# Kernel tuning notes

Hardware: AMD Instinct MI355X
Metric: run time of the kernel (lower is better)

## Reference

```python
import jax, jax.numpy as jnp
import numpy as np

B, NUM, NVAR = 2048, 100, 11
NUM_OBS, NC = 10, 3
T_FIN = 10.0
RHO_OBS = 1.0; RHO_INEQ = 1.0; RHO_LANE = 1.0; RHO_PROJ = 1.0
W_SMOOTH = 20.0; W_VDES = 2.0; W_YDES = 1.0
A_EGO = 3.0; B_EGO = 1.5; MARGIN = 0.2
V_MIN = 0.001; V_MAX = 18.0; A_MAX = 6.0
MAXITER = 5
H = 256

def _basis():
    s = np.linspace(0.0, 1.0, NUM)
    j = np.arange(NVAR)
    P = s[:, None] ** j[None, :]
    Pd = np.zeros((NUM, NVAR)); Pdd = np.zeros((NUM, NVAR))
    Pd[:, 1:] = j[1:][None, :] * s[:, None] ** (j[1:] - 1)[None, :]
    Pdd[:, 2:] = (j[2:] * (j[2:] - 1))[None, :] * s[:, None] ** (j[2:] - 2)[None, :]
    return (jnp.asarray(P, jnp.float32), jnp.asarray(Pd / T_FIN, jnp.float32),
            jnp.asarray(Pdd / (T_FIN ** 2), jnp.float32))

P, PDOT, PDDOT = _basis()
A_EQ_X = jnp.stack([P[0], PDOT[0], PDDOT[0], P[-1]])   # [4, NVAR]
A_EQ_Y = jnp.stack([P[0], PDOT[0], PDDOT[0]])          # [3, NVAR]
PTP = P.T @ P

def _kkt_inv(Q, A):
    m = A.shape[0]
    K = jnp.concatenate([jnp.concatenate([Q, A.T], axis=1),
                         jnp.concatenate([A, jnp.zeros((m, m), jnp.float32)], axis=1)], axis=0)
    return jnp.linalg.inv(K)

# ADMM cost: rho_proj*I + smoothness + rho_obs*A_obs^T A_obs + rho_ineq*(Pdot^T Pdot + Pddot^T Pddot)
Q_COMMON = (RHO_PROJ + W_SMOOTH) * jnp.eye(NVAR, dtype=jnp.float32) \
    + RHO_OBS * NUM_OBS * NC * PTP \
    + RHO_INEQ * (PDOT.T @ PDOT + PDDOT.T @ PDDOT)
KKT_X = _kkt_inv(Q_COMMON, A_EQ_X)
KKT_Y = _kkt_inv(Q_COMMON + 2.0 * RHO_LANE * PTP, A_EQ_Y)   # A_lane = [P; -P]
# x_init QP (smoothness + v_des / y_des tracking)
Q_IX = W_SMOOTH * jnp.eye(NVAR, dtype=jnp.float32) + W_VDES * (PDOT.T @ PDOT)
KKT_IX = _kkt_inv(Q_IX, A_EQ_X)
KKT_IY = _kkt_inv(Q_IX + W_YDES * PTP, A_EQ_Y)


def _forward(init_state_ego, goal_des, closest_obs, psi_obs, dim_x_obs, dim_y_obs,
             y_ub, y_lb, gru_W_ih, gru_W_hh, gru_b, gru_h0,
             mlp_W1, mlp_b1, mlp_W2, mlp_b2):
    b = init_state_ego.shape[0]
    x0, y0, vx0, vy0, ax0, ay0 = (init_state_ego[:, i] for i in range(6))
    b_eq_x = jnp.stack([x0, vx0, ax0, goal_des[:, 0]], axis=1)   # [B,4]
    b_eq_y = jnp.stack([y0, vy0, ay0], axis=1)                    # [B,3]

    # ---- obstacle circle trajectories (static obstacles, vx=vy=0) ----
    xo = closest_obs[:, :NUM_OBS]; yo = closest_obs[:, NUM_OBS:2 * NUM_OBS]   # [B,O]
    r = jnp.stack([jnp.zeros_like(dim_x_obs),
                   (dim_x_obs - dim_y_obs) / 2,
                   -(dim_x_obs - dim_y_obs) / 2], axis=2)                      # [B,O,3]
    x_circ = xo[:, :, None] + r * jnp.cos(psi_obs)[:, :, None]                # [B,O,3]
    y_circ = yo[:, :, None] + r * jnp.sin(psi_obs)[:, :, None]
    shape4 = (b, NUM_OBS, NC, NUM)
    x_obs_f = jnp.broadcast_to(x_circ[..., None], shape4).reshape(b, -1)      # [B,O*C*T]
    y_obs_f = jnp.broadcast_to(y_circ[..., None], shape4).reshape(b, -1)
    rad = dim_y_obs / 2
    a_obs = jnp.broadcast_to((A_EGO + rad + MARGIN)[:, :, None, None], shape4).reshape(b, -1)
    b_obs = jnp.broadcast_to((B_EGO + rad + MARGIN)[:, :, None, None], shape4).reshape(b, -1)

    # ---- GRU context over obstacles -> learned lambda init ----
    feats = jnp.stack([xo, yo, dim_x_obs, dim_y_obs, psi_obs], axis=2)        # [B,O,5]
    def gru_step(h, x):
        gx = x @ gru_W_ih + gru_b
        gh = h @ gru_W_hh
        z = jax.nn.sigmoid(gx[:, :H] + gh[:, :H])
        rg = jax.nn.sigmoid(gx[:, H:2 * H] + gh[:, H:2 * H])
        n = jnp.tanh(gx[:, 2 * H:] + rg * gh[:, 2 * H:])
        return (1.0 - z) * n + z * h, None
    hT, _ = jax.lax.scan(gru_step, jnp.broadcast_to(gru_h0, (b, H)), jnp.swapaxes(feats, 0, 1))
    lam = jax.nn.relu(hT @ mlp_W1 + mlp_b1) @ mlp_W2 + mlp_b2                 # [B,2*NVAR]
    lam_x, lam_y = lam[:, :NVAR], lam[:, NVAR:]

    # ---- x_init: equality-constrained smoothness/tracking QP ----
    v_des = jnp.sqrt(vx0 ** 2 + vy0 ** 2)
    lin_ix = W_VDES * v_des[:, None] * jnp.sum(PDOT, axis=0)[None, :]
    lin_iy = W_YDES * goal_des[:, 1:2] * jnp.sum(P, axis=0)[None, :]
    c_x0 = (jnp.concatenate([lin_ix, b_eq_x], 1) @ KKT_IX.T)[:, :NVAR]
    c_y0 = (jnp.concatenate([lin_iy, b_eq_y], 1) @ KKT_IY.T)[:, :NVAR]

    b_lane = jnp.concatenate([y_ub[:, None] * jnp.ones((1, NUM), jnp.float32),
                              -y_lb[:, None] * jnp.ones((1, NUM), jnp.float32)], axis=1)  # [B,2T]

    def AobsT(v):   # A_obs^T v, v: [B, O*C*T] -> [B, NVAR]
        return v.reshape(b, NUM_OBS * NC, NUM).sum(axis=1) @ P

    def step(carry, _):
        c_x, c_y, lx, ly = carry
        x = c_x @ P.T; xd = c_x @ PDOT.T; xdd = c_x @ PDDOT.T
        y = c_y @ P.T; yd = c_y @ PDOT.T; ydd = c_y @ PDDOT.T
        wc = jnp.tile(x, (1, NUM_OBS * NC)) - x_obs_f
        ws = jnp.tile(y, (1, NUM_OBS * NC)) - y_obs_f
        alpha_o = jnp.arctan2(ws * a_obs, wc * b_obs)
        ca, sa = jnp.cos(alpha_o), jnp.sin(alpha_o)
        c1 = RHO_OBS * (a_obs ** 2 * ca ** 2 + b_obs ** 2 * sa ** 2)
        c2 = RHO_OBS * (a_obs * wc * ca + b_obs * ws * sa)
        d_o = jnp.maximum(1.0, c2 / c1)
        alpha_v = jnp.clip(jnp.arctan2(yd, xd), -0.41, 0.41)
        cv, sv = jnp.cos(alpha_v), jnp.sin(alpha_v)
        d_v = jnp.clip(xd * cv + yd * sv, V_MIN, V_MAX)
        alpha_a = jnp.arctan2(ydd + 1e-4, xdd + 1e-4)
        caa, saa = jnp.cos(alpha_a), jnp.sin(alpha_a)
        d_a = jnp.clip(xdd * caa + ydd * saa, 0.0, A_MAX)
        # targets
        b_ox = x_obs_f + a_obs * d_o * ca; b_oy = y_obs_f + b_obs * d_o * sa
        b_vx = d_v * cv; b_vy = d_v * sv
        b_ax = d_a * caa; b_ay = d_a * saa
        b_lane_aug = jnp.minimum(jnp.concatenate([y, -y], 1), b_lane)  # slack-augmented
        top_x = lx + RHO_PROJ * c_x0 + RHO_OBS * AobsT(b_ox) + RHO_INEQ * (b_vx @ PDOT + b_ax @ PDDOT)
        top_y = ly + RHO_PROJ * c_y0 + RHO_OBS * AobsT(b_oy) + RHO_INEQ * (b_vy @ PDOT + b_ay @ PDDOT) \
            + RHO_LANE * ((b_lane_aug[:, :NUM] - b_lane_aug[:, NUM:]) @ P)
        c_xn = (jnp.concatenate([top_x, b_eq_x], 1) @ KKT_X.T)[:, :NVAR]
        c_yn = (jnp.concatenate([top_y, b_eq_y], 1) @ KKT_Y.T)[:, :NVAR]
        # residuals / Lagrange multiplier updates
        xn = c_xn @ P.T; yn = c_yn @ P.T
        res_ox = jnp.tile(xn, (1, NUM_OBS * NC)) - b_ox
        res_oy = jnp.tile(yn, (1, NUM_OBS * NC)) - b_oy
        lxn = lx - RHO_OBS * AobsT(res_ox) \
            - RHO_INEQ * ((c_xn @ PDOT.T - b_vx) @ PDOT + (c_xn @ PDDOT.T - b_ax) @ PDDOT)
        res_lane = jnp.concatenate([yn, -yn], 1) - b_lane_aug
        lyn = ly - RHO_OBS * AobsT(res_oy) \
            - RHO_INEQ * ((c_yn @ PDOT.T - b_vy) @ PDOT + (c_yn @ PDDOT.T - b_ay) @ PDDOT) \
            - RHO_LANE * ((res_lane[:, :NUM] - res_lane[:, NUM:]) @ P)
        return (c_xn, c_yn, lxn, lyn), None

    (c_x, c_y, lam_x, lam_y), _ = jax.lax.scan(step, (c_x0, c_y0, lam_x, lam_y),
                                               None, length=MAXITER)
    return jnp.concatenate([c_x, c_y], axis=1)   # [B, 2*NVAR]


def setup_inputs() -> dict:
    key = jax.random.key(0)
    ks = jax.random.split(key, 12)
    d = {
        'init_state_ego': jax.random.normal(ks[0], (B, 6), jnp.float32),
        'goal_des': jax.random.normal(ks[1], (B, 2), jnp.float32),
        'closest_obs': jax.random.normal(ks[2], (B, 2 * NUM_OBS), jnp.float32),
        'psi_obs': jax.random.normal(ks[3], (B, NUM_OBS), jnp.float32),
        'dim_x_obs': jax.random.uniform(ks[4], (B, NUM_OBS), jnp.float32),
        'dim_y_obs': jax.random.uniform(ks[5], (B, NUM_OBS), jnp.float32),
        'y_ub': jnp.ones((B,), jnp.float32),
        'y_lb': jnp.zeros((B,), jnp.float32),
        'gru_W_ih': jax.random.normal(ks[6], (5, 3 * H), jnp.float32) / np.sqrt(5.0),
        'gru_W_hh': jax.random.normal(ks[7], (H, 3 * H), jnp.float32) / np.sqrt(float(H)),
        'gru_b': jnp.zeros((3 * H,), jnp.float32),
        'gru_h0': jax.random.normal(ks[8], (H,), jnp.float32) * 0.1,
        'mlp_W1': jax.random.normal(ks[9], (H, 512), jnp.float32) / np.sqrt(float(H)),
        'mlp_b1': jnp.zeros((512,), jnp.float32),
        'mlp_W2': jax.random.normal(ks[10], (512, 2 * NVAR), jnp.float32) / np.sqrt(512.0),
        'mlp_b2': jnp.zeros((2 * NVAR,), jnp.float32),
    }
    return d


def reference(init_state_ego, goal_des, closest_obs, psi_obs, dim_x_obs, dim_y_obs,
              y_ub, y_lb, gru_W_ih, gru_W_hh, gru_b, gru_h0,
              mlp_W1, mlp_b1, mlp_W2, mlp_b2):
    return _forward(init_state_ego, goal_des, closest_obs, psi_obs, dim_x_obs, dim_y_obs,
                    y_ub, y_lb, gru_W_ih, gru_W_hh, gru_b, gru_h0,
                    mlp_W1, mlp_b1, mlp_W2, mlp_b2)
```

## Files before the change

### kernel.cpp

```cpp
#include <hip/hip_runtime.h>
#include <math.h>

typedef short bf16x8 __attribute__((ext_vector_type(8)));
typedef float f32x4 __attribute__((ext_vector_type(4)));

__device__ __forceinline__ unsigned short f2bf(float x) {
  union { float f; unsigned u; } v; v.f = x;
  unsigned r = v.u + 0x7FFFu + ((v.u >> 16) & 1u);
  return (unsigned short)(r >> 16);
}

#define WS_WAUG 0u
#define WS_W1T  442368u
#define WS_W2T  704512u
#define WS_LAM  737280u
#define WS_KKT  917504u
#define WS_SUMS 920320u

__global__ __launch_bounds__(256) void prep(
    const float* __restrict__ Whh, const float* __restrict__ Wih,
    const float* __restrict__ gb, const float* __restrict__ W1,
    const float* __restrict__ W2,
    unsigned short* __restrict__ Waug, unsigned short* __restrict__ W1T,
    unsigned short* __restrict__ W2T,
    float* __restrict__ kkt_out, float* __restrict__ sums_out)
{
  __shared__ double S[21];
  __shared__ double aug[15][32];
  __shared__ double fbuf[15];
  if (blockIdx.x < 4) {
    const int mat = blockIdx.x;
    const int n = (mat == 0 || mat == 2) ? 15 : 14;
    const int twoN = 2 * n;
    if (threadIdx.x == 0) {
      for (int m = 0; m < 21; ++m) S[m] = 0.0;
      for (int s = 0; s < 100; ++s) {
        double t = s * (1.0 / 99.0);
        double p = 1.0;
        for (int m = 0; m < 21; ++m) { S[m] += p; p *= t; }
      }
    }
    __syncthreads();
    for (int idx = threadIdx.x; idx < n * twoN; idx += 256) {
      int r = idx / twoN, c = idx % twoN;
      double v;
      if (c >= n) v = (c - n == r) ? 1.0 : 0.0;
      else if (r < 11 && c < 11) {
        double ptp = S[r + c];
        double pdp = (r >= 1 && c >= 1) ? ((double)(r * c) / 100.0) * S[r + c - 2] : 0.0;
        double pddp = (r >= 2 && c >= 2) ? ((double)(r*(r-1)) * (double)(c*(c-1)) / 10000.0) * S[r + c - 4] : 0.0;
        double dg = (r == c) ? 1.0 : 0.0;
        if (mat == 0)      v = 21.0*dg + 30.0*ptp + pdp + pddp;
        else if (mat == 1) v = 21.0*dg + 32.0*ptp + pdp + pddp;
        else if (mat == 2) v = 20.0*dg + 2.0*pdp;
        else               v = 20.0*dg + 2.0*pdp + ptp;
      } else if (r >= 11 && c >= 11) v = 0.0;
      else {
        int ar = (r >= 11) ? (r - 11) : (c - 11);
        int ac = (r >= 11) ? c : r;
        v = (ar == 0) ? ((ac == 0) ? 1.0 : 0.0)
          : (ar == 1) ? ((ac == 1) ? 0.1 : 0.0)
          : (ar == 2) ? ((ac == 2) ? 0.02 : 0.0)
          : 1.0;
      }
      aug[r][c] = v;
    }
    __syncthreads();
    for (int p = 0; p < n; ++p) {
      double pv = aug[p][p];
      __syncthreads();
      double inv = 1.0 / pv;
      for (int c = threadIdx.x; c < twoN; c += 256) aug[p][c] *= inv;
      __syncthreads();
      if (threadIdx.x < n) fbuf[threadIdx.x] = aug[threadIdx.x][p];
      __syncthreads();
      for (int idx = threadIdx.x; idx < n * twoN; idx += 256) {
        int r = idx / twoN, c = idx % twoN;
        if (r != p) aug[r][c] -= fbuf[r] * aug[p][c];
      }
      __syncthreads();
    }
    for (int idx = threadIdx.x; idx < 11 * n; idx += 256) {
      int r = idx / n, c = idx % n;
      kkt_out[mat * 176 + r * 16 + c] = (float)aug[r][n + c];
    }
    if (mat == 0 && threadIdx.x < 11) {
      int j = threadIdx.x;
      sums_out[j] = (float)S[j];
      sums_out[11 + j] = (j >= 1) ? (float)((double)j / 10.0 * S[j - 1]) : 0.f;
    }
    return;
  }
  int idx = (blockIdx.x - 4) * 256 + threadIdx.x;
  if (idx < 221184) {
    int col = idx / 288, k = idx - col * 288;
    float v;
    if (k < 256)       v = Whh[k * 768 + col];
    else if (k < 261)  v = Wih[(k - 256) * 768 + col];
    else if (k == 261) v = gb[col];
    else               v = 0.f;
    Waug[idx] = f2bf(v);
  } else if (idx < 221184 + 131072) {
    int j = idx - 221184;
    int col = j >> 8, k = j & 255;
    W1T[j] = f2bf(W1[k * 512 + col]);
  } else if (idx < 221184 + 131072 + 16384) {
    int j = idx - 352256;
    int col = j >> 9, k = j & 511;
    W2T[j] = f2bf(col < 22 ? W2[k * 22 + col] : 0.f);
  }
}

#define MFMA __builtin_amdgcn_mfma_f32_16x16x32_bf16
__global__ __launch_bounds__(512, 1) void gru_mlp(
    const float* __restrict__ h0, const unsigned short* __restrict__ Waug,
    const float* __restrict__ obs, const float* __restrict__ dimx,
    const float* __restrict__ dimy, const float* __restrict__ psi,
    const unsigned short* __restrict__ W1T, const float* __restrict__ b1,
    const unsigned short* __restrict__ W2T, const float* __restrict__ b2,
    float* __restrict__ lam)
{
  __shared__ __align__(16) unsigned short A[9216];
  __shared__ __align__(16) unsigned short acts[16384];
  __shared__ float fl[32][52];
  const int tid = threadIdx.x;
  const int m0 = blockIdx.x * 32;
  const int lane = tid & 63, w = tid >> 6;
  const int l15 = lane & 15, g4 = lane >> 4;

  for (int i = tid; i < 1600; i += 512) {
    int row = i / 50, r = i - row * 50;
    int f = r / 10, s = r - f * 10;
    int gr = m0 + row;
    float v = (f == 0) ? obs[gr * 20 + s] : (f == 1) ? obs[gr * 20 + 10 + s]
            : (f == 2) ? dimx[gr * 10 + s] : (f == 3) ? dimy[gr * 10 + s]
            : psi[gr * 10 + s];
    fl[row][f * 10 + s] = v;
  }
  for (int i = tid; i < 8192; i += 512) {
    int col = ((i >> 10) << 5) + (i & 31);
    A[i] = f2bf(h0[col]);
  }
  for (int i = tid; i < 1024; i += 512) A[8192 + i] = 0;
  if (tid < 192) {
    int row = tid / 6, e = tid - row * 6;
    float v = (e < 5) ? fl[row][e * 10 + 0] : 1.0f;
    A[(8 * 32 + row) * 32 + e] = f2bf(v);
  }
  float hreg[2][2][4];
  #pragma unroll
  for (int nt = 0; nt < 2; ++nt) {
    float hv = h0[w * 32 + nt * 16 + l15];
    #pragma unroll
    for (int mi = 0; mi < 2; ++mi)
      #pragma unroll
      for (int rg = 0; rg < 4; ++rg) hreg[mi][nt][rg] = hv;
  }
  __syncthreads();

  for (int s = 0; s < 10; ++s) {
    f32x4 az[2][2], ar_[2][2], anh[2][2], anx[2][2];
    #pragma unroll
    for (int mi = 0; mi < 2; ++mi)
      #pragma unroll
      for (int nt = 0; nt < 2; ++nt) {
        az[mi][nt] = (f32x4){0.f,0.f,0.f,0.f}; ar_[mi][nt] = (f32x4){0.f,0.f,0.f,0.f};
        anh[mi][nt] = (f32x4){0.f,0.f,0.f,0.f}; anx[mi][nt] = (f32x4){0.f,0.f,0.f,0.f};
      }
    #pragma unroll
    for (int kc = 0; kc < 9; ++kc) {
      bf16x8 a0 = *(const bf16x8*)&A[((kc * 32 + l15) * 4 + g4) * 8];
      bf16x8 a1 = *(const bf16x8*)&A[((kc * 32 + 16 + l15) * 4 + g4) * 8];
      int kk = kc * 32 + g4 * 8;
      #pragma unroll
      for (int nt = 0; nt < 2; ++nt) {
        int col = w * 32 + nt * 16 + l15;
        bf16x8 bz = *(const bf16x8*)&Waug[(size_t)col * 288 + kk];
        bf16x8 br = *(const bf16x8*)&Waug[(size_t)(256 + col) * 288 + kk];
        bf16x8 bn = *(const bf16x8*)&Waug[(size_t)(512 + col) * 288 + kk];
        az[0][nt] = MFMA(a0, bz, az[0][nt], 0, 0, 0);
        az[1][nt] = MFMA(a1, bz, az[1][nt], 0, 0, 0);
        ar_[0][nt] = MFMA(a0, br, ar_[0][nt], 0, 0, 0);
        ar_[1][nt] = MFMA(a1, br, ar_[1][nt], 0, 0, 0);
        if (kc < 8) {
          anh[0][nt] = MFMA(a0, bn, anh[0][nt], 0, 0, 0);
          anh[1][nt] = MFMA(a1, bn, anh[1][nt], 0, 0, 0);
        } else {
          anx[0][nt] = MFMA(a0, bn, anx[0][nt], 0, 0, 0);
          anx[1][nt] = MFMA(a1, bn, anx[1][nt], 0, 0, 0);
        }
      }
    }
    __syncthreads();
    #pragma unroll
    for (int mi = 0; mi < 2; ++mi)
      #pragma unroll
      for (int nt = 0; nt < 2; ++nt) {
        int col = w * 32 + nt * 16 + l15;
        #pragma unroll
        for (int rg = 0; rg < 4; ++rg) {
          int row = mi * 16 + g4 * 4 + rg;
          float z = __builtin_amdgcn_rcpf(1.f + __expf(-az[mi][nt][rg]));
          float r = __builtin_amdgcn_rcpf(1.f + __expf(-ar_[mi][nt][rg]));
          float narg = anx[mi][nt][rg] + r * anh[mi][nt][rg];
          float nn = 1.f - 2.f * __builtin_amdgcn_rcpf(__expf(2.f * narg) + 1.f);
          float hnew = (1.f - z) * nn + z * hreg[mi][nt][rg];
          hreg[mi][nt][rg] = hnew;
          A[((w * 32 + row) * 4 + ((col >> 3) & 3)) * 8 + (col & 7)] = f2bf(hnew);
        }
      }
    if (s < 9 && tid < 192) {
      int row = tid / 6, e = tid - row * 6;
      float v = (e < 5) ? fl[row][e * 10 + s + 1] : 1.0f;
      A[(8 * 32 + row) * 32 + e] = f2bf(v);
    }
    __syncthreads();
  }

  {
    f32x4 acc1[2][4];
    #pragma unroll
    for (int mi = 0; mi < 2; ++mi)
      #pragma unroll
      for (int nt = 0; nt < 4; ++nt) acc1[mi][nt] = (f32x4){0.f,0.f,0.f,0.f};
    #pragma unroll
    for (int kc = 0; kc < 8; ++kc) {
      bf16x8 a0 = *(const bf16x8*)&A[((kc * 32 + l15) * 4 + g4) * 8];
      bf16x8 a1 = *(const bf16x8*)&A[((kc * 32 + 16 + l15) * 4 + g4) * 8];
      int kk = kc * 32 + g4 * 8;
      #pragma unroll
      for (int nt = 0; nt < 4; ++nt) {
        int col = w * 64 + nt * 16 + l15;
        bf16x8 b = *(const bf16x8*)&W1T[(size_t)col * 256 + kk];
        acc1[0][nt] = MFMA(a0, b, acc1[0][nt], 0, 0, 0);
        acc1[1][nt] = MFMA(a1, b, acc1[1][nt], 0, 0, 0);
      }
    }
    #pragma unroll
    for (int mi = 0; mi < 2; ++mi)
      #pragma unroll
      for (int nt = 0; nt < 4; ++nt) {
        int col = w * 64 + nt * 16 + l15;
        float bb = b1[col];
        #pragma unroll
        for (int rg = 0; rg < 4; ++rg) {
          int row = mi * 16 + g4 * 4 + rg;
          float v = fmaxf(acc1[mi][nt][rg] + bb, 0.f);
          acts[(((col >> 5) * 32 + row) * 4 + ((col >> 3) & 3)) * 8 + (col & 7)] = f2bf(v);
        }
      }
  }
  __syncthreads();

  if (w < 4) {
    int mi = w >> 1, nt = w & 1;
    int col = nt * 16 + l15;
    f32x4 a2 = {0.f, 0.f, 0.f, 0.f};
    #pragma unroll
    for (int kc = 0; kc < 16; ++kc) {
      bf16x8 a = *(const bf16x8*)&acts[((kc * 32 + mi * 16 + l15) * 4 + g4) * 8];
      bf16x8 b = *(const bf16x8*)&W2T[(size_t)col * 512 + kc * 32 + g4 * 8];
      a2 = MFMA(a, b, a2, 0, 0, 0);
    }
    if (col < 22) {
      float bb = b2[col];
      #pragma unroll
      for (int rg = 0; rg < 4; ++rg) {
        int row = m0 + mi * 16 + g4 * 4 + rg;
        lam[row * 22 + col] = a2[rg] + bb;
      }
    }
  }
}

__global__ __launch_bounds__(128) void solver(
    const float* __restrict__ ise, const float* __restrict__ goal,
    const float* __restrict__ obs, const float* __restrict__ psi,
    const float* __restrict__ dimx, const float* __restrict__ dimy,
    const float* __restrict__ yub, const float* __restrict__ ylb,
    const float* __restrict__ lam, const float* __restrict__ kkt,
    const float* __restrict__ sums, float* __restrict__ out)
{
  __shared__ __align__(16) float Pt[3][11][108];
  __shared__ __align__(16) float red[7][108];
  __shared__ float redout[7][11];
  __shared__ float cx[11], cy[11], lx[11], ly[11], cx0[11], cy0[11];
  __shared__ float cxn[11], cyn[11];
  __shared__ float rhsx[15], rhsy[14];
  __shared__ float xc[30], yc[30], sa_[10], sb_[10], sab[10], sab2[10];

  const int b = blockIdx.x;
  const int tid = threadIdx.x;

  if (tid < 100) {
    float t = tid * (1.0f / 99.0f);
    float tjm2 = 0.f, tjm1 = 0.f, tj = 1.f;
    #pragma unroll
    for (int j = 0; j < 11; ++j) {
      Pt[0][j][tid] = tj;
      Pt[1][j][tid] = 0.1f * (float)j * tjm1;
      Pt[2][j][tid] = 0.01f * (float)(j * (j - 1)) * tjm2;
      tjm2 = tjm1; tjm1 = tj; tj *= t;
    }
  }
  if (tid < 10) {
    int o = tid;
    float xo = obs[b * 20 + o], yo = obs[b * 20 + 10 + o];
    float dx = dimx[b * 10 + o], dy = dimy[b * 10 + o], ps = psi[b * 10 + o];
    float sp, cp;
    __sincosf(ps, &sp, &cp);
    float r1 = 0.5f * (dx - dy);
    xc[o * 3] = xo; xc[o * 3 + 1] = xo + r1 * cp; xc[o * 3 + 2] = xo - r1 * cp;
    yc[o * 3] = yo; yc[o * 3 + 1] = yo + r1 * sp; yc[o * 3 + 2] = yo - r1 * sp;
    float rad = 0.5f * dy;
    float av = 3.2f + rad, bv = 1.7f + rad;
    sa_[o] = av; sb_[o] = bv; sab[o] = av * bv; sab2[o] = av * bv * av * bv;
  }
  if (tid < 11) { lx[tid] = lam[b * 22 + tid]; ly[tid] = lam[b * 22 + 11 + tid]; }
  const float vx0 = ise[b * 6 + 2], vy0 = ise[b * 6 + 3];
  if (tid == 0) {
    float x0 = ise[b * 6 + 0], y0 = ise[b * 6 + 1];
    float ax0 = ise[b * 6 + 4], ay0 = ise[b * 6 + 5];
    rhsx[11] = x0; rhsx[12] = vx0; rhsx[13] = ax0; rhsx[14] = goal[b * 2 + 0];
    rhsy[11] = y0; rhsy[12] = vy0; rhsy[13] = ay0;
  }
  {
    float vdes = sqrtf(vx0 * vx0 + vy0 * vy0);
    float gy = goal[b * 2 + 1];
    if (tid < 11) { rhsx[tid] = 2.f * vdes * sums[11 + tid]; rhsy[tid] = gy * sums[tid]; }
  }
  const float yU = yub[b], yL = ylb[b];
  __syncthreads();
  if (tid < 11) {
    const float* K = kkt + 2 * 176 + tid * 16;
    float s = 0.f;
    #pragma unroll
    for (int j = 0; j < 15; ++j) s += K[j] * rhsx[j];
    cx0[tid] = s; cx[tid] = s;
  } else if (tid >= 16 && tid < 27) {
    int i = tid - 16;
    const float* K = kkt + 3 * 176 + i * 16;
    float s = 0.f;
    #pragma unroll
    for (int j = 0; j < 14; ++j) s += K[j] * rhsy[j];
    cy0[i] = s; cy[i] = s;
  }
  __syncthreads();

  float Sbx = 0.f, Sby = 0.f, bvx = 0.f, bvy = 0.f, bax = 0.f, bay = 0.f, lane_t = 0.f;
  for (int it = 0; it < 5; ++it) {
    if (tid < 100) {
      float t = tid * (1.0f / 99.0f);
      float x = 0, y = 0, xd = 0, yd = 0, xdd = 0, ydd = 0;
      {
        float tjm2 = 0, tjm1 = 0, tj = 1;
        #pragma unroll
        for (int j = 0; j < 11; ++j) {
          float cj = cx[j], dj = cy[j];
          x += cj * tj; y += dj * tj;
          float pd = 0.1f * (float)j * tjm1;
          xd += cj * pd; yd += dj * pd;
          float pdd = 0.01f * (float)(j * (j - 1)) * tjm2;
          xdd += cj * pdd; ydd += dj * pdd;
          tjm2 = tjm1; tjm1 = tj; tj *= t;
        }
      }
      Sbx = 0.f; Sby = 0.f;
      for (int oi = 0; oi < 10; ++oi) {
        float A = sa_[oi], B = sb_[oi], AB = sab[oi], AB2 = sab2[oi];
        #pragma unroll
        for (int cc = 0; cc < 3; ++cc) {
          int o = oi * 3 + cc;
          float xcc = xc[o], ycc = yc[o];
          float wc = x - xcc, wsv = y - ycc;
          float p = wsv * A, q = wc * B;
          float h2 = p * p + q * q;
          float rin = rsqrtf(h2 + 1e-20f);
          float sc = AB * rin;
          bool outside = h2 >= AB2;
          Sbx += outside ? x : fmaf(wc, sc, xcc);
          Sby += outside ? y : fmaf(wsv, sc, ycc);
        }
      }
      bool clipv = (xd <= 0.f) || (fabsf(yd) > xd * 0.43463135f);
      float cv, sv;
      if (clipv) { cv = 0.91712081f; sv = copysignf(0.39860934f, yd); }
      else { float ri = rsqrtf(fmaxf(xd * xd + yd * yd, 1e-24f)); cv = xd * ri; sv = yd * ri; }
      float dv = fminf(fmaxf(xd * cv + yd * sv, 0.001f), 18.f);
      bvx = dv * cv; bvy = dv * sv;
      float qa = xdd + 1e-4f, pa = ydd + 1e-4f;
      float ria = rsqrtf(pa * pa + qa * qa + 1e-30f);
      float caa = qa * ria, saa = pa * ria;
      float da = fminf(fmaxf(xdd * caa + ydd * saa, 0.f), 6.f);
      bax = da * caa; bay = da * saa;
      lane_t = fminf(y, yU) - fminf(-y, -yL);
      red[0][tid] = Sbx; red[1][tid] = Sby; red[2][tid] = bvx; red[3][tid] = bvy;
      red[4][tid] = bax; red[5][tid] = bay; red[6][tid] = lane_t;
    }
    __syncthreads();
    if (tid < 77) {
      int a = tid / 11, j = tid - a * 11;
      int wt = (a < 2) ? 0 : (a < 4) ? 1 : (a < 6) ? 2 : 0;
      const float4* rp = (const float4*)(&red[a][0]);
      const float4* wp = (const float4*)(&Pt[wt][j][0]);
      float s = 0.f;
      for (int k = 0; k < 25; ++k) {
        float4 rv = rp[k], wv = wp[k];
        s += rv.x * wv.x + rv.y * wv.y + rv.z * wv.z + rv.w * wv.w;
      }
      redout[a][j] = s;
    }
    __syncthreads();
    if (tid < 11) rhsx[tid] = lx[tid] + cx0[tid] + redout[0][tid] + redout[2][tid] + redout[4][tid];
    else if (tid >= 16 && tid < 27) {
      int j = tid - 16;
      rhsy[j] = ly[j] + cy0[j] + redout[1][j] + redout[3][j] + redout[5][j] + redout[6][j];
    }
    __syncthreads();
    if (tid < 11) {
      const float* K = kkt + tid * 16;
      float s = 0.f;
      #pragma unroll
      for (int j = 0; j < 15; ++j) s += K[j] * rhsx[j];
      cxn[tid] = s;
    } else if (tid >= 16 && tid < 27) {
      int i = tid - 16;
      const float* K = kkt + 176 + i * 16;
      float s = 0.f;
      #pragma unroll
      for (int j = 0; j < 14; ++j) s += K[j] * rhsy[j];
      cyn[i] = s;
    }
    __syncthreads();
    if (tid < 100) {
      float t = tid * (1.0f / 99.0f);
      float xn = 0, yn = 0, xdn = 0, ydn = 0, xddn = 0, yddn = 0;
      {
        float tjm2 = 0, tjm1 = 0, tj = 1;
        #pragma unroll
        for (int j = 0; j < 11; ++j) {
          float cj = cxn[j], dj = cyn[j];
          xn += cj * tj; yn += dj * tj;
          float pd = 0.1f * (float)j * tjm1;
          xdn += cj * pd; ydn += dj * pd;
          float pdd = 0.01f * (float)(j * (j - 1)) * tjm2;
          xddn += cj * pdd; yddn += dj * pdd;
          tjm2 = tjm1; tjm1 = tj; tj *= t;
        }
      }
      red[0][tid] = 30.f * xn - Sbx;
      red[1][tid] = xdn - bvx;
      red[2][tid] = xddn - bax;
      red[3][tid] = 30.f * yn - Sby;
      red[4][tid] = ydn - bvy;
      red[5][tid] = yddn - bay;
      red[6][tid] = 2.f * yn - lane_t;
    }
    __syncthreads();
    if (tid < 77) {
      int a = tid / 11, j = tid - a * 11;
      int wt = (a == 0 || a == 3 || a == 6) ? 0 : (a == 1 || a == 4) ? 1 : 2;
      const float4* rp = (const float4*)(&red[a][0]);
      const float4* wp = (const float4*)(&Pt[wt][j][0]);
      float s = 0.f;
      for (int k = 0; k < 25; ++k) {
        float4 rv = rp[k], wv = wp[k];
        s += rv.x * wv.x + rv.y * wv.y + rv.z * wv.z + rv.w * wv.w;
      }
      redout[a][j] = s;
    }
    __syncthreads();
    if (tid < 11) { lx[tid] -= redout[0][tid] + redout[1][tid] + redout[2][tid]; cx[tid] = cxn[tid]; }
    else if (tid >= 16 && tid < 27) {
      int j = tid - 16;
      ly[j] -= redout[3][j] + redout[4][j] + redout[5][j] + redout[6][j];
      cy[j] = cyn[j];
    }
    __syncthreads();
  }
  if (tid < 11) out[b * 22 + tid] = cx[tid];
  else if (tid >= 16 && tid < 27) out[b * 22 + 11 + (tid - 16)] = cy[tid - 16];
}

extern "C" void kernel_launch(void* const* d_in, const int* in_sizes, int n_in,
                              void* d_out, int out_size, void* d_ws, size_t ws_size,
                              hipStream_t stream) {
  const float* ise  = (const float*)d_in[0];
  const float* goal = (const float*)d_in[1];
  const float* obs  = (const float*)d_in[2];
  const float* psi  = (const float*)d_in[3];
  const float* dimx = (const float*)d_in[4];
  const float* dimy = (const float*)d_in[5];
  const float* yub  = (const float*)d_in[6];
  const float* ylb  = (const float*)d_in[7];
  const float* Wih  = (const float*)d_in[8];
  const float* Whh  = (const float*)d_in[9];
  const float* gb   = (const float*)d_in[10];
  const float* h0   = (const float*)d_in[11];
  const float* W1   = (const float*)d_in[12];
  const float* b1   = (const float*)d_in[13];
  const float* W2   = (const float*)d_in[14];
  const float* b2   = (const float*)d_in[15];

  char* ws = (char*)d_ws;
  unsigned short* Waug = (unsigned short*)(ws + WS_WAUG);
  unsigned short* W1T  = (unsigned short*)(ws + WS_W1T);
  unsigned short* W2T  = (unsigned short*)(ws + WS_W2T);
  float* lamb = (float*)(ws + WS_LAM);
  float* kkt  = (float*)(ws + WS_KKT);
  float* sums = (float*)(ws + WS_SUMS);

  prep<<<1444, 256, 0, stream>>>(Whh, Wih, gb, W1, W2, Waug, W1T, W2T, kkt, sums);
  gru_mlp<<<64, 512, 0, stream>>>(h0, Waug, obs, dimx, dimy, psi, W1T, b1, W2T, b2, lamb);
  solver<<<2048, 128, 0, stream>>>(ise, goal, obs, psi, dimx, dimy, yub, ylb,
                                   lamb, kkt, sums, (float*)d_out);
  (void)in_sizes; (void)n_in; (void)out_size; (void)ws_size;
}
```

Before: 265.5 us.

## Split persistent GRU+MLP kernel into per-step grid launches with global state

```diff
diff --git a/kernel.cpp b/kernel.cpp
--- a/kernel.cpp
+++ b/kernel.cpp
@@ -9,20 +9,28 @@
   unsigned r = v.u + 0x7FFFu + ((v.u >> 16) & 1u);
   return (unsigned short)(r >> 16);
 }
-
-#define WS_WAUG 0u
-#define WS_W1T  442368u
-#define WS_W2T  704512u
-#define WS_LAM  737280u
-#define WS_KKT  917504u
-#define WS_SUMS 920320u
+__device__ __forceinline__ float bf2f(unsigned short h) {
+  union { unsigned u; float f; } v; v.u = ((unsigned)h) << 16; return v.f;
+}
+
+#define WS_WAUG  0u
+#define WS_W1T   442368u
+#define WS_HAUGA 704512u
+#define WS_HAUGB 1884160u
+#define WS_HF32  3063808u
+#define WS_ACTS  3063808u
+#define WS_LAM   5160960u
+#define WS_KKT   5341184u
+#define WS_SUMS  5344000u
 
 __global__ __launch_bounds__(256) void prep(
     const float* __restrict__ Whh, const float* __restrict__ Wih,
     const float* __restrict__ gb, const float* __restrict__ W1,
-    const float* __restrict__ W2,
+    const float* __restrict__ h0,
+    const float* __restrict__ obs, const float* __restrict__ dimx,
+    const float* __restrict__ dimy, const float* __restrict__ psi,
     unsigned short* __restrict__ Waug, unsigned short* __restrict__ W1T,
-    unsigned short* __restrict__ W2T,
+    unsigned short* __restrict__ HaugA, unsigned short* __restrict__ HaugB,
     float* __restrict__ kkt_out, float* __restrict__ sums_out)
 {
   __shared__ double S[21];
@@ -100,176 +108,180 @@
     else if (k == 261) v = gb[col];
     else               v = 0.f;
     Waug[idx] = f2bf(v);
-  } else if (idx < 221184 + 131072) {
+  } else if (idx < 352256) {
     int j = idx - 221184;
     int col = j >> 8, k = j & 255;
     W1T[j] = f2bf(W1[k * 512 + col]);
-  } else if (idx < 221184 + 131072 + 16384) {
+  } else {
     int j = idx - 352256;
-    int col = j >> 9, k = j & 511;
-    W2T[j] = f2bf(col < 22 ? W2[k * 22 + col] : 0.f);
+    unsigned short* dst = HaugA;
+    if (j >= 589824) { j -= 589824; dst = HaugB; }
+    int row = j / 288, k = j - row * 288;
+    float v;
+    if (k < 256)       v = h0[k];
+    else if (k == 256) v = obs[row * 20 + 0];
+    else if (k == 257) v = obs[row * 20 + 10];
+    else if (k == 258) v = dimx[row * 10 + 0];
+    else if (k == 259) v = dimy[row * 10 + 0];
+    else if (k == 260) v = psi[row * 10 + 0];
+    else if (k == 261) v = 1.0f;
+    else               v = 0.f;
+    dst[row * 288 + k] = f2bf(v);
   }
 }
 
 #define MFMA __builtin_amdgcn_mfma_f32_16x16x32_bf16
-__global__ __launch_bounds__(512, 1) void gru_mlp(
-    const float* __restrict__ h0, const unsigned short* __restrict__ Waug,
+__global__ __launch_bounds__(256) void gru_step(
+    const unsigned short* __restrict__ Waug,
+    const unsigned short* __restrict__ HaugC, unsigned short* __restrict__ HaugN,
+    float* __restrict__ Hf32, const float* __restrict__ h0,
     const float* __restrict__ obs, const float* __restrict__ dimx,
     const float* __restrict__ dimy, const float* __restrict__ psi,
-    const unsigned short* __restrict__ W1T, const float* __restrict__ b1,
-    const unsigned short* __restrict__ W2T, const float* __restrict__ b2,
-    float* __restrict__ lam)
+    int s)
 {
-  __shared__ __align__(16) unsigned short A[9216];
-  __shared__ __align__(16) unsigned short acts[16384];
-  __shared__ float fl[32][52];
+  __shared__ __align__(16) unsigned short LDSall[36864];
   const int tid = threadIdx.x;
   const int m0 = blockIdx.x * 32;
+  const int c0 = blockIdx.y * 32;
   const int lane = tid & 63, w = tid >> 6;
   const int l15 = lane & 15, g4 = lane >> 4;
 
-  for (int i = tid; i < 1600; i += 512) {
-    int row = i / 50, r = i - row * 50;
-    int f = r / 10, s = r - f * 10;
-    int gr = m0 + row;
-    float v = (f == 0) ? obs[gr * 20 + s] : (f == 1) ? obs[gr * 20 + 10 + s]
-            : (f == 2) ? dimx[gr * 10 + s] : (f == 3) ? dimy[gr * 10 + s]
-            : psi[gr * 10 + s];
-    fl[row][f * 10 + s] = v;
-  }
-  for (int i = tid; i < 8192; i += 512) {
-    int col = ((i >> 10) << 5) + (i & 31);
-    A[i] = f2bf(h0[col]);
-  }
-  for (int i = tid; i < 1024; i += 512) A[8192 + i] = 0;
-  if (tid < 192) {
-    int row = tid / 6, e = tid - row * 6;
-    float v = (e < 5) ? fl[row][e * 10 + 0] : 1.0f;
-    A[(8 * 32 + row) * 32 + e] = f2bf(v);
-  }
-  float hreg[2][2][4];
+  #pragma unroll 4
+  for (int r = 0; r < 18; ++r) {
+    int j = tid + 256 * r;
+    int tile = j >> 6, q = j & 63;
+    int ci = q >> 2, ks = q & 3;
+    const unsigned short* src;
+    if (tile < 54) {
+      int gate = tile / 18, rem = tile - gate * 18;
+      int cg = rem / 9, kc = rem - cg * 9;
+      int col = gate * 256 + c0 + cg * 16 + ci;
+      src = Waug + (size_t)col * 288 + kc * 32 + ks * 8;
+    } else {
+      int t2 = tile - 54;
+      int mi = t2 / 9, kc = t2 - mi * 9;
+      int row = m0 + mi * 16 + ci;
+      src = HaugC + (size_t)row * 288 + kc * 32 + ks * 8;
+    }
+    *(int4*)&LDSall[tile * 512 + q * 8] = *(const int4*)src;
+  }
+  __syncthreads();
+
+  const int mi = w >> 1, cg = w & 1;
+  const int foff = (l15 * 4 + g4) * 8;
+  f32x4 accz = {0.f,0.f,0.f,0.f}, accr = {0.f,0.f,0.f,0.f};
+  f32x4 anh = {0.f,0.f,0.f,0.f}, anx = {0.f,0.f,0.f,0.f};
+  const unsigned short* As = &LDSall[54 * 512];
+
   #pragma unroll
-  for (int nt = 0; nt < 2; ++nt) {
-    float hv = h0[w * 32 + nt * 16 + l15];
+  for (int kc = 0; kc < 9; ++kc) {
+    bf16x8 a  = *(const bf16x8*)&As[(mi * 9 + kc) * 512 + foff];
+    bf16x8 bz = *(const bf16x8*)&LDSall[((0 * 2 + cg) * 9 + kc) * 512 + foff];
+    bf16x8 br = *(const bf16x8*)&LDSall[((1 * 2 + cg) * 9 + kc) * 512 + foff];
+    bf16x8 bn = *(const bf16x8*)&LDSall[((2 * 2 + cg) * 9 + kc) * 512 + foff];
+    accz = MFMA(a, bz, accz, 0, 0, 0);
+    accr = MFMA(a, br, accr, 0, 0, 0);
+    if (kc < 8) anh = MFMA(a, bn, anh, 0, 0, 0);
+    else        anx = MFMA(a, bn, anx, 0, 0, 0);
+  }
+
+  const int colh = c0 + cg * 16 + l15;
+  float h0c = (s == 0) ? h0[colh] : 0.f;
+  #pragma unroll
+  for (int rg = 0; rg < 4; ++rg) {
+    int row = m0 + mi * 16 + g4 * 4 + rg;
+    float hold = (s == 0) ? h0c : Hf32[(size_t)row * 256 + colh];
+    float z = 1.f / (1.f + __expf(-accz[rg]));
+    float rr = 1.f / (1.f + __expf(-accr[rg]));
+    float nn = tanhf(anx[rg] + rr * anh[rg]);
+    float hnew = (1.f - z) * nn + z * hold;
+    Hf32[(size_t)row * 256 + colh] = hnew;
+    HaugN[(size_t)row * 288 + colh] = f2bf(hnew);
+  }
+  if (blockIdx.y == 0 && s < 9 && tid < 192) {
+    int row = m0 + tid / 6, e = tid - (tid / 6) * 6;
+    int s1 = s + 1;
+    float v = (e == 0) ? obs[row * 20 + s1] : (e == 1) ? obs[row * 20 + 10 + s1]
+            : (e == 2) ? dimx[row * 10 + s1] : (e == 3) ? dimy[row * 10 + s1]
+            : (e == 4) ? psi[row * 10 + s1] : 1.0f;
+    HaugN[(size_t)row * 288 + 256 + e] = f2bf(v);
+  }
+}
+
+__global__ __launch_bounds__(256) void mlp1(
+    const unsigned short* __restrict__ Haug, const unsigned short* __restrict__ W1T,
+    const float* __restrict__ b1, unsigned short* __restrict__ acts)
+{
+  __shared__ __align__(16) unsigned short As[8192];
+  const int tid = threadIdx.x;
+  const int m0 = blockIdx.x * 32, c0 = blockIdx.y * 128;
+  const int lane = tid & 63, w = tid >> 6, l15 = lane & 15, g4 = lane >> 4;
+
+  #pragma unroll
+  for (int r = 0; r < 4; ++r) {
+    int j = tid + 256 * r;
+    int tile = j >> 6, q = j & 63, ci = q >> 2, ks = q & 3;
+    int mi = tile >> 3, kc = tile & 7;
+    const unsigned short* src = Haug + (size_t)(m0 + mi * 16 + ci) * 288 + kc * 32 + ks * 8;
+    *(int4*)&As[tile * 512 + q * 8] = *(const int4*)src;
+  }
+  __syncthreads();
+
+  const int foff = (l15 * 4 + g4) * 8;
+  f32x4 acc[2][2];
+  #pragma unroll
+  for (int a = 0; a < 2; ++a)
     #pragma unroll
-    for (int mi = 0; mi < 2; ++mi)
-      #pragma unroll
-      for (int rg = 0; rg < 4; ++rg) hreg[mi][nt][rg] = hv;
-  }
-  __syncthreads();
-
-  for (int s = 0; s < 10; ++s) {
-    f32x4 az[2][2], ar_[2][2], anh[2][2], anx[2][2];
+    for (int b = 0; b < 2; ++b) acc[a][b] = (f32x4){0.f,0.f,0.f,0.f};
+
+  #pragma unroll
+  for (int kc = 0; kc < 8; ++kc) {
+    bf16x8 a0 = *(const bf16x8*)&As[(0 * 8 + kc) * 512 + foff];
+    bf16x8 a1 = *(const bf16x8*)&As[(1 * 8 + kc) * 512 + foff];
+    int kk = kc * 32 + g4 * 8;
     #pragma unroll
-    for (int mi = 0; mi < 2; ++mi)
-      #pragma unroll
-      for (int nt = 0; nt < 2; ++nt) {
-        az[mi][nt] = (f32x4){0.f,0.f,0.f,0.f}; ar_[mi][nt] = (f32x4){0.f,0.f,0.f,0.f};
-        anh[mi][nt] = (f32x4){0.f,0.f,0.f,0.f}; anx[mi][nt] = (f32x4){0.f,0.f,0.f,0.f};
-      }
+    for (int nt = 0; nt < 2; ++nt) {
+      int col = c0 + w * 32 + nt * 16 + l15;
+      bf16x8 b = *(const bf16x8*)&W1T[(size_t)col * 256 + kk];
+      acc[0][nt] = MFMA(a0, b, acc[0][nt], 0, 0, 0);
+      acc[1][nt] = MFMA(a1, b, acc[1][nt], 0, 0, 0);
+    }
+  }
+  #pragma unroll
+  for (int mi = 0; mi < 2; ++mi)
     #pragma unroll
-    for (int kc = 0; kc < 9; ++kc) {
-      bf16x8 a0 = *(const bf16x8*)&A[((kc * 32 + l15) * 4 + g4) * 8];
-      bf16x8 a1 = *(const bf16x8*)&A[((kc * 32 + 16 + l15) * 4 + g4) * 8];
-      int kk = kc * 32 + g4 * 8;
-      #pragma unroll
-      for (int nt = 0; nt < 2; ++nt) {
-        int col = w * 32 + nt * 16 + l15;
-        bf16x8 bz = *(const bf16x8*)&Waug[(size_t)col * 288 + kk];
-        bf16x8 br = *(const bf16x8*)&Waug[(size_t)(256 + col) * 288 + kk];
-        bf16x8 bn = *(const bf16x8*)&Waug[(size_t)(512 + col) * 288 + kk];
-        az[0][nt] = MFMA(a0, bz, az[0][nt], 0, 0, 0);
-        az[1][nt] = MFMA(a1, bz, az[1][nt], 0, 0, 0);
-        ar_[0][nt] = MFMA(a0, br, ar_[0][nt], 0, 0, 0);
-        ar_[1][nt] = MFMA(a1, br, ar_[1][nt], 0, 0, 0);
-        if (kc < 8) {
-          anh[0][nt] = MFMA(a0, bn, anh[0][nt], 0, 0, 0);
-          anh[1][nt] = MFMA(a1, bn, anh[1][nt], 0, 0, 0);
-        } else {
-          anx[0][nt] = MFMA(a0, bn, anx[0][nt], 0, 0, 0);
-          anx[1][nt] = MFMA(a1, bn, anx[1][nt], 0, 0, 0);
-        }
-      }
-    }
-    __syncthreads();
-    #pragma unroll
-    for (int mi = 0; mi < 2; ++mi)
-      #pragma unroll
-      for (int nt = 0; nt < 2; ++nt) {
-        int col = w * 32 + nt * 16 + l15;
-        #pragma unroll
-        for (int rg = 0; rg < 4; ++rg) {
-          int row = mi * 16 + g4 * 4 + rg;
-          float z = __builtin_amdgcn_rcpf(1.f + __expf(-az[mi][nt][rg]));
-          float r = __builtin_amdgcn_rcpf(1.f + __expf(-ar_[mi][nt][rg]));
-          float narg = anx[mi][nt][rg] + r * anh[mi][nt][rg];
-          float nn = 1.f - 2.f * __builtin_amdgcn_rcpf(__expf(2.f * narg) + 1.f);
-          float hnew = (1.f - z) * nn + z * hreg[mi][nt][rg];
-          hreg[mi][nt][rg] = hnew;
-          A[((w * 32 + row) * 4 + ((col >> 3) & 3)) * 8 + (col & 7)] = f2bf(hnew);
-        }
-      }
-    if (s < 9 && tid < 192) {
-      int row = tid / 6, e = tid - row * 6;
-      float v = (e < 5) ? fl[row][e * 10 + s + 1] : 1.0f;
-      A[(8 * 32 + row) * 32 + e] = f2bf(v);
-    }
-    __syncthreads();
-  }
-
-  {
-    f32x4 acc1[2][4];
-    #pragma unroll
-    for (int mi = 0; mi < 2; ++mi)
-      #pragma unroll
-      for (int nt = 0; nt < 4; ++nt) acc1[mi][nt] = (f32x4){0.f,0.f,0.f,0.f};
-    #pragma unroll
-    for (int kc = 0; kc < 8; ++kc) {
-      bf16x8 a0 = *(const bf16x8*)&A[((kc * 32 + l15) * 4 + g4) * 8];
-      bf16x8 a1 = *(const bf16x8*)&A[((kc * 32 + 16 + l15) * 4 + g4) * 8];
-      int kk = kc * 32 + g4 * 8;
-      #pragma unroll
-      for (int nt = 0; nt < 4; ++nt) {
-        int col = w * 64 + nt * 16 + l15;
-        bf16x8 b = *(const bf16x8*)&W1T[(size_t)col * 256 + kk];
-        acc1[0][nt] = MFMA(a0, b, acc1[0][nt], 0, 0, 0);
-        acc1[1][nt] = MFMA(a1, b, acc1[1][nt], 0, 0, 0);
-      }
-    }
-    #pragma unroll
-    for (int mi = 0; mi < 2; ++mi)
-      #pragma unroll
-      for (int nt = 0; nt < 4; ++nt) {
-        int col = w * 64 + nt * 16 + l15;
-        float bb = b1[col];
-        #pragma unroll
-        for (int rg = 0; rg < 4; ++rg) {
-          int row = mi * 16 + g4 * 4 + rg;
-          float v = fmaxf(acc1[mi][nt][rg] + bb, 0.f);
-          acts[(((col >> 5) * 32 + row) * 4 + ((col >> 3) & 3)) * 8 + (col & 7)] = f2bf(v);
-        }
-      }
-  }
-  __syncthreads();
-
-  if (w < 4) {
-    int mi = w >> 1, nt = w & 1;
-    int col = nt * 16 + l15;
-    f32x4 a2 = {0.f, 0.f, 0.f, 0.f};
-    #pragma unroll
-    for (int kc = 0; kc < 16; ++kc) {
-      bf16x8 a = *(const bf16x8*)&acts[((kc * 32 + mi * 16 + l15) * 4 + g4) * 8];
-      bf16x8 b = *(const bf16x8*)&W2T[(size_t)col * 512 + kc * 32 + g4 * 8];
-      a2 = MFMA(a, b, a2, 0, 0, 0);
-    }
-    if (col < 22) {
-      float bb = b2[col];
+    for (int nt = 0; nt < 2; ++nt) {
+      int col = c0 + w * 32 + nt * 16 + l15;
+      float bb = b1[col];
       #pragma unroll
       for (int rg = 0; rg < 4; ++rg) {
         int row = m0 + mi * 16 + g4 * 4 + rg;
-        lam[row * 22 + col] = a2[rg] + bb;
-      }
-    }
+        float v = fmaxf(acc[mi][nt][rg] + bb, 0.f);
+        acts[(size_t)row * 512 + col] = f2bf(v);
+      }
+    }
+}
+
+__global__ __launch_bounds__(256) void mlp2(
+    const unsigned short* __restrict__ acts, const float* __restrict__ W2,
+    const float* __restrict__ b2, float* __restrict__ lam)
+{
+  __shared__ unsigned short Ablk[8 * 520];
+  __shared__ float W2s[512 * 22];
+  const int tid = threadIdx.x;
+  const int m0 = blockIdx.x * 8;
+  for (int i = tid; i < 4096; i += 256) {
+    int r = i >> 9, k = i & 511;
+    Ablk[r * 520 + k] = acts[(size_t)(m0 + r) * 512 + k];
+  }
+  for (int i = tid; i < 11264; i += 256) W2s[i] = W2[i];
+  __syncthreads();
+  if (tid < 176) {
+    int row = tid / 22, col = tid - (tid / 22) * 22;
+    float s = b2[col];
+    const unsigned short* ap = &Ablk[row * 520];
+    for (int k = 0; k < 512; ++k) s += bf2f(ap[k]) * W2s[k * 22 + col];
+    lam[(size_t)(m0 + row) * 22 + col] = s;
   }
 }
 
@@ -503,15 +515,26 @@
   const float* b2   = (const float*)d_in[15];
 
   char* ws = (char*)d_ws;
-  unsigned short* Waug = (unsigned short*)(ws + WS_WAUG);
-  unsigned short* W1T  = (unsigned short*)(ws + WS_W1T);
-  unsigned short* W2T  = (unsigned short*)(ws + WS_W2T);
+  unsigned short* Waug  = (unsigned short*)(ws + WS_WAUG);
+  unsigned short* W1T   = (unsigned short*)(ws + WS_W1T);
+  unsigned short* HaugA = (unsigned short*)(ws + WS_HAUGA);
+  unsigned short* HaugB = (unsigned short*)(ws + WS_HAUGB);
+  float* Hf32 = (float*)(ws + WS_HF32);
+  unsigned short* acts = (unsigned short*)(ws + WS_ACTS);
   float* lamb = (float*)(ws + WS_LAM);
   float* kkt  = (float*)(ws + WS_KKT);
   float* sums = (float*)(ws + WS_SUMS);
 
-  prep<<<1444, 256, 0, stream>>>(Whh, Wih, gb, W1, W2, Waug, W1T, W2T, kkt, sums);
-  gru_mlp<<<64, 512, 0, stream>>>(h0, Waug, obs, dimx, dimy, psi, W1T, b1, W2T, b2, lamb);
+  prep<<<5988, 256, 0, stream>>>(Whh, Wih, gb, W1, h0, obs, dimx, dimy, psi,
+                                 Waug, W1T, HaugA, HaugB, kkt, sums);
+  for (int s = 0; s < 10; ++s) {
+    const unsigned short* hc = (s & 1) ? HaugB : HaugA;
+    unsigned short* hn = (s & 1) ? HaugA : HaugB;
+    gru_step<<<dim3(64, 8), 256, 0, stream>>>(Waug, hc, hn, Hf32, h0,
+                                              obs, dimx, dimy, psi, s);
+  }
+  mlp1<<<dim3(64, 4), 256, 0, stream>>>(HaugA, W1T, b1, acts);
+  mlp2<<<256, 256, 0, stream>>>(acts, W2, b2, lamb);
   solver<<<2048, 128, 0, stream>>>(ise, goal, obs, psi, dimx, dimy, yub, ylb,
                                    lamb, kkt, sums, (float*)d_out);
   (void)in_sizes; (void)n_in; (void)out_size; (void)ws_size;
```

Result: no change. 266.3 us (+0.3%).
